# Optimization experiments

Hardware: AMD Instinct MI355X
Metric: run time of the kernel (lower is better)

## Reference

```python
import jax, jax.numpy as jnp
import numpy as np

XYZ, DIRS, APP = 63, 27, 0
HID, OUT, NLAYERS, SKIPS = 256, 4, 8, (4,)

def _linear_init(key, fan_in, fan_out):
    kw, kb = jax.random.split(key)
    s = 1.0 / np.sqrt(fan_in)
    W = jax.random.uniform(kw, (fan_in, fan_out), jnp.float32, -s, s)
    b = jax.random.uniform(kb, (fan_out,), jnp.float32, -s, s)
    return W, b

def setup_inputs() -> dict:
    key = jax.random.key(0)
    keys = jax.random.split(key, NLAYERS + 2)
    x = jax.random.normal(keys[0], (262144, XYZ + DIRS + APP), jnp.float32)
    d = {"x": x}
    in_dim = XYZ
    for i in range(NLAYERS):
        # skip-concat: layer after a skip index sees hid+xyz inputs
        fan_in = HID + XYZ if (i - 1) in SKIPS else (XYZ if i == 0 else HID)
        W, b = _linear_init(keys[i + 1], fan_in, HID)
        d[f"W{i}"], d[f"b{i}"] = W, b
    Wout, bout = _linear_init(keys[-1], HID, OUT)
    d["Wout"], d["bout"] = Wout, bout
    return d

def reference(x, W0, b0, W1, b1, W2, b2, W3, b3, W4, b4, W5, b5, W6, b6, W7, b7, Wout, bout):
    Ws = [W0, W1, W2, W3, W4, W5, W6, W7]
    bs = [b0, b1, b2, b3, b4, b5, b6, b7]
    input_pts = x[..., :XYZ]  # dirs/app split off but unused (use_viewdirs=False)
    h = input_pts
    for i in range(NLAYERS):
        h = jax.nn.relu(h @ Ws[i] + bs[i])
        if i in SKIPS:
            h = jnp.concatenate([input_pts, h], axis=-1)
    return h @ Wout + bout  # [N, 4] = rgb + density logits
```

## Files before the change

### kernel.cpp

```cpp
#include <hip/hip_runtime.h>


typedef _Float16 h8 __attribute__((ext_vector_type(8)));
typedef float f4 __attribute__((ext_vector_type(4)));

#define OFF_L0   0
#define OFF_L1   16384
#define OFF_L2   81920
#define OFF_L3   147456
#define OFF_L4   212992
#define OFF_L5   278528
#define OFF_L6   360448
#define OFF_L7   425984
#define OFF_OUT  491520
#define TOT_HALVES 495616
#define TOT_GROUPS (TOT_HALVES / 8)

__global__ void nerf_prep(const float* __restrict__ W0, const float* __restrict__ W1,
                          const float* __restrict__ W2, const float* __restrict__ W3,
                          const float* __restrict__ W4, const float* __restrict__ W5,
                          const float* __restrict__ W6, const float* __restrict__ W7,
                          const float* __restrict__ Wout, _Float16* __restrict__ wf)
{
    int g = blockIdx.x * 256 + threadIdx.x;
    if (g >= TOT_GROUPS) return;

    const int bounds[10] = {0, 2048, 10240, 18432, 26624, 34816, 45056, 53248, 61440, 61952};
    const float* Ws[9] = {W0, W1, W2, W3, W4, W5, W6, W7, Wout};

    int L = 0;
    while (L < 8 && g >= bounds[L + 1]) ++L;

    int t    = g - bounds[L];
    int lane = t & 63;
    int q    = t >> 6;
    int NF   = (L == 8) ? 1 : 16;
    int nf   = q % NF;
    int ks   = q / NF;
    int n    = nf * 16 + (lane & 15);
    int k0   = ks * 32 + (lane >> 4) * 8;

    const float* W = Ws[L];
    h8 v;
#pragma unroll
    for (int i = 0; i < 8; ++i) {
        int k = k0 + i;
        float val = 0.f;
        if (L == 0) {
            if (k < 63) val = W[k * 256 + n];
        } else if (L == 5) {
            if (k < 256)            val = W[(63 + k) * 256 + n];
            else if ((k - 256) < 63) val = W[(k - 256) * 256 + n];
        } else if (L == 8) {
            if (n < 4) val = W[k * 4 + n];
        } else {
            val = W[k * 256 + n];
        }
        v[i] = (_Float16)val;
    }
    *(h8*)(wf + (size_t)g * 8) = v;
}

__device__ __forceinline__ const h8* bfrag_ptr(const _Float16* __restrict__ w,
                                               int ks, int wid, int nf, int lane)
{
    return (const h8*)(w + (size_t)((ks * 16 + (wid * 4 + nf)) * 64 + lane) * 8);
}

__device__ __forceinline__ void barrier_nodrain()
{
    asm volatile("s_waitcnt lgkmcnt(0)" ::: "memory");
    __builtin_amdgcn_s_barrier();
    __builtin_amdgcn_sched_barrier(0);
}

template <int KSTEPS, int MODE, int GB3, bool LAST>
__device__ __forceinline__ void mlp_layer(_Float16 (&hbuf)[64][264], _Float16 (&xbuf)[64][72],
                                          const _Float16* __restrict__ wfrag,
                                          const _Float16* __restrict__ wnext,
                                          const float* __restrict__ bias,
                                          int wid, int lane, h8 (&pf)[3][4])
{
    const int lg = lane >> 4, ln = lane & 15;

    f4 bv[4];
#pragma unroll
    for (int cf = 0; cf < 4; ++cf)
        bv[cf] = *(const f4*)&bias[wid * 64 + cf * 16 + lg * 4];

    f4 acc[4][4];
#pragma unroll
    for (int cf = 0; cf < 4; ++cf)
#pragma unroll
        for (int sf = 0; sf < 4; ++sf)
            acc[cf][sf] = bv[cf];

#pragma unroll
    for (int ks = 0; ks < KSTEPS; ++ks) {
        const int slot = (GB3 + ks) % 3;
        __builtin_amdgcn_s_setprio(1);
        h8 hfr[4];
#pragma unroll
        for (int sf = 0; sf < 4; ++sf) {
            const _Float16* ap;
            if constexpr (MODE == 1) {
                ap = &xbuf[sf * 16 + ln][ks * 32 + lg * 8];
            } else if constexpr (MODE == 2) {
                ap = (ks < 8) ? &hbuf[sf * 16 + ln][ks * 32 + lg * 8]
                              : &xbuf[sf * 16 + ln][(ks - 8) * 32 + lg * 8];
            } else {
                ap = &hbuf[sf * 16 + ln][ks * 32 + lg * 8];
            }
            hfr[sf] = *(const h8*)ap;
        }
#pragma unroll
        for (int cf = 0; cf < 4; ++cf)
#pragma unroll
            for (int sf = 0; sf < 4; ++sf)
                acc[cf][sf] = __builtin_amdgcn_mfma_f32_16x16x32_f16(pf[slot][cf], hfr[sf], acc[cf][sf], 0, 0, 0);
        __builtin_amdgcn_s_setprio(0);
        if (ks + 3 < KSTEPS) {
#pragma unroll
            for (int cf = 0; cf < 4; ++cf)
                pf[slot][cf] = *bfrag_ptr(wfrag, ks + 3, wid, cf, lane);
        } else if (!LAST) {
#pragma unroll
            for (int cf = 0; cf < 4; ++cf)
                pf[slot][cf] = *bfrag_ptr(wnext, ks + 3 - KSTEPS, wid, cf, lane);
        }
    }

    barrier_nodrain();

#pragma unroll
    for (int cf = 0; cf < 4; ++cf) {
#pragma unroll
        for (int sf = 0; sf < 4; ++sf) {
            union { _Float16 h[4]; unsigned long long u; } p;
#pragma unroll
            for (int i = 0; i < 4; ++i)
                p.h[i] = (_Float16)fmaxf(acc[cf][sf][i], 0.f);
            *(unsigned long long*)&hbuf[sf * 16 + ln][wid * 64 + cf * 16 + lg * 4] = p.u;
        }
    }
    barrier_nodrain();
}

__global__ __launch_bounds__(256, 3) void nerf_fused(
    const float* __restrict__ x,
    const float* __restrict__ b0, const float* __restrict__ b1, const float* __restrict__ b2,
    const float* __restrict__ b3, const float* __restrict__ b4, const float* __restrict__ b5,
    const float* __restrict__ b6, const float* __restrict__ b7, const float* __restrict__ bout,
    const _Float16* __restrict__ wf,
    float* __restrict__ out)
{
    __shared__ _Float16 hbuf[64][264];
    __shared__ _Float16 xbuf[64][72];

    const int tid  = threadIdx.x;
    const int wid  = tid >> 6;
    const int lane = tid & 63;
    const int lg   = lane >> 4, ln = lane & 15;
    const int row0 = blockIdx.x * 64;

    h8 pf[3][4];
#pragma unroll
    for (int cf = 0; cf < 4; ++cf) {
        pf[0][cf] = *bfrag_ptr(wf + OFF_L0, 0, wid, cf, lane);
        pf[1][cf] = *bfrag_ptr(wf + OFF_L0, 1, wid, cf, lane);
        pf[2][cf] = *bfrag_ptr(wf + OFF_L1, 0, wid, cf, lane);
    }

    for (int idx = tid; idx < 64 * 64; idx += 256) {
        int r = idx >> 6, c = idx & 63;
        float v = (c < 63) ? x[(size_t)(row0 + r) * 90 + c] : 0.f;
        xbuf[r][c] = (_Float16)v;
    }
    barrier_nodrain();

    mlp_layer<2,  1, 0, false>(hbuf, xbuf, wf + OFF_L0, wf + OFF_L1, b0, wid, lane, pf);
    mlp_layer<8,  0, 2, false>(hbuf, xbuf, wf + OFF_L1, wf + OFF_L2, b1, wid, lane, pf);
    mlp_layer<8,  0, 1, false>(hbuf, xbuf, wf + OFF_L2, wf + OFF_L3, b2, wid, lane, pf);
    mlp_layer<8,  0, 0, false>(hbuf, xbuf, wf + OFF_L3, wf + OFF_L4, b3, wid, lane, pf);
    mlp_layer<8,  0, 2, false>(hbuf, xbuf, wf + OFF_L4, wf + OFF_L5, b4, wid, lane, pf);
    mlp_layer<10, 2, 1, false>(hbuf, xbuf, wf + OFF_L5, wf + OFF_L6, b5, wid, lane, pf);
    mlp_layer<8,  0, 2, false>(hbuf, xbuf, wf + OFF_L6, wf + OFF_L7, b6, wid, lane, pf);
    mlp_layer<8,  0, 1, true >(hbuf, xbuf, wf + OFF_L7, wf + OFF_L7, b7, wid, lane, pf);

    f4 oacc;
#pragma unroll
    for (int i = 0; i < 4; ++i) oacc[i] = 0.f;
#pragma unroll
    for (int ks = 0; ks < 8; ++ks) {
        h8 bfr = *(const h8*)(wf + OFF_OUT + (size_t)(ks * 64 + lane) * 8);
        h8 afr = *(const h8*)&hbuf[wid * 16 + ln][ks * 32 + lg * 8];
        oacc = __builtin_amdgcn_mfma_f32_16x16x32_f16(afr, bfr, oacc, 0, 0, 0);
    }
    if (ln < 4) {
        float bo = bout[ln];
#pragma unroll
        for (int i = 0; i < 4; ++i) {
            int r = row0 + wid * 16 + lg * 4 + i;
            out[(size_t)r * 4 + ln] = oacc[i] + bo;
        }
    }
}

extern "C" void kernel_launch(void* const* d_in, const int* in_sizes, int n_in,
                              void* d_out, int out_size, void* d_ws, size_t ws_size,
                              hipStream_t stream)
{
    const float* x = (const float*)d_in[0];
    const float* W[9];
    const float* b[9];
    for (int i = 0; i < 8; ++i) {
        W[i] = (const float*)d_in[1 + 2 * i];
        b[i] = (const float*)d_in[2 + 2 * i];
    }
    W[8] = (const float*)d_in[17];
    b[8] = (const float*)d_in[18];

    _Float16* wf = (_Float16*)d_ws;

    nerf_prep<<<(TOT_GROUPS + 255) / 256, 256, 0, stream>>>(
        W[0], W[1], W[2], W[3], W[4], W[5], W[6], W[7], W[8], wf);

    nerf_fused<<<262144 / 64, 256, 0, stream>>>(
        x, b[0], b[1], b[2], b[3], b[4], b[5], b[6], b[7], b[8], wf,
        (float*)d_out);
}
```

Before: 234.9 us.

## Ping-pong activation buffers to drop the mid-layer barrier

Activations now alternate between two shared-memory buffers per layer, so each layer reads one and writes the other. This removes the barrier between a layer's MFMA reads and its writeback. Layer 0 reads only xbuf, so it writes hb[0] in place, and the output head reads hb[1]. The doubled LDS footprint lowers the occupancy hint from 3 to 2 blocks per CU, which cuts latency hiding in exchange for one fewer barrier per layer.

New measurement: 241.2 us. +2.7%, slower.

```diff
diff --git a/kernel.cpp b/kernel.cpp
--- a/kernel.cpp
+++ b/kernel.cpp
@@ -49,7 +49,7 @@
         if (L == 0) {
             if (k < 63) val = W[k * 256 + n];
         } else if (L == 5) {
-            if (k < 256)            val = W[(63 + k) * 256 + n];
+            if (k < 256)             val = W[(63 + k) * 256 + n];
             else if ((k - 256) < 63) val = W[(k - 256) * 256 + n];
         } else if (L == 8) {
             if (n < 4) val = W[k * 4 + n];
@@ -75,7 +75,9 @@
 }
 
 template <int KSTEPS, int MODE, int GB3, bool LAST>
-__device__ __forceinline__ void mlp_layer(_Float16 (&hbuf)[64][264], _Float16 (&xbuf)[64][72],
+__device__ __forceinline__ void mlp_layer(const _Float16 (&rbuf)[64][264],
+                                          _Float16 (&wbuf)[64][264],
+                                          const _Float16 (&xbuf)[64][72],
                                           const _Float16* __restrict__ wfrag,
                                           const _Float16* __restrict__ wnext,
                                           const float* __restrict__ bias,
@@ -106,10 +108,10 @@
             if constexpr (MODE == 1) {
                 ap = &xbuf[sf * 16 + ln][ks * 32 + lg * 8];
             } else if constexpr (MODE == 2) {
-                ap = (ks < 8) ? &hbuf[sf * 16 + ln][ks * 32 + lg * 8]
+                ap = (ks < 8) ? &rbuf[sf * 16 + ln][ks * 32 + lg * 8]
                               : &xbuf[sf * 16 + ln][(ks - 8) * 32 + lg * 8];
             } else {
-                ap = &hbuf[sf * 16 + ln][ks * 32 + lg * 8];
+                ap = &rbuf[sf * 16 + ln][ks * 32 + lg * 8];
             }
             hfr[sf] = *(const h8*)ap;
         }
@@ -123,14 +125,14 @@
 #pragma unroll
             for (int cf = 0; cf < 4; ++cf)
                 pf[slot][cf] = *bfrag_ptr(wfrag, ks + 3, wid, cf, lane);
-        } else if (!LAST) {
-#pragma unroll
-            for (int cf = 0; cf < 4; ++cf)
-                pf[slot][cf] = *bfrag_ptr(wnext, ks + 3 - KSTEPS, wid, cf, lane);
-        }
-    }
-
-    barrier_nodrain();
+        } else {
+            if constexpr (!LAST) {
+#pragma unroll
+                for (int cf = 0; cf < 4; ++cf)
+                    pf[slot][cf] = *bfrag_ptr(wnext, ks + 3 - KSTEPS, wid, cf, lane);
+            }
+        }
+    }
 
 #pragma unroll
     for (int cf = 0; cf < 4; ++cf) {
@@ -140,13 +142,13 @@
 #pragma unroll
             for (int i = 0; i < 4; ++i)
                 p.h[i] = (_Float16)fmaxf(acc[cf][sf][i], 0.f);
-            *(unsigned long long*)&hbuf[sf * 16 + ln][wid * 64 + cf * 16 + lg * 4] = p.u;
+            *(unsigned long long*)&wbuf[sf * 16 + ln][wid * 64 + cf * 16 + lg * 4] = p.u;
         }
     }
     barrier_nodrain();
 }
 
-__global__ __launch_bounds__(256, 3) void nerf_fused(
+__global__ __launch_bounds__(256, 2) void nerf_fused(
     const float* __restrict__ x,
     const float* __restrict__ b0, const float* __restrict__ b1, const float* __restrict__ b2,
     const float* __restrict__ b3, const float* __restrict__ b4, const float* __restrict__ b5,
@@ -154,7 +156,7 @@
     const _Float16* __restrict__ wf,
     float* __restrict__ out)
 {
-    __shared__ _Float16 hbuf[64][264];
+    __shared__ _Float16 hb[2][64][264];
     __shared__ _Float16 xbuf[64][72];
 
     const int tid  = threadIdx.x;
@@ -178,14 +180,14 @@
     }
     barrier_nodrain();
 
-    mlp_layer<2,  1, 0, false>(hbuf, xbuf, wf + OFF_L0, wf + OFF_L1, b0, wid, lane, pf);
-    mlp_layer<8,  0, 2, false>(hbuf, xbuf, wf + OFF_L1, wf + OFF_L2, b1, wid, lane, pf);
-    mlp_layer<8,  0, 1, false>(hbuf, xbuf, wf + OFF_L2, wf + OFF_L3, b2, wid, lane, pf);
-    mlp_layer<8,  0, 0, false>(hbuf, xbuf, wf + OFF_L3, wf + OFF_L4, b3, wid, lane, pf);
-    mlp_layer<8,  0, 2, false>(hbuf, xbuf, wf + OFF_L4, wf + OFF_L5, b4, wid, lane, pf);
-    mlp_layer<10, 2, 1, false>(hbuf, xbuf, wf + OFF_L5, wf + OFF_L6, b5, wid, lane, pf);
-    mlp_layer<8,  0, 2, false>(hbuf, xbuf, wf + OFF_L6, wf + OFF_L7, b6, wid, lane, pf);
-    mlp_layer<8,  0, 1, true >(hbuf, xbuf, wf + OFF_L7, wf + OFF_L7, b7, wid, lane, pf);
+    mlp_layer<2,  1, 0, false>(hb[0], hb[0], xbuf, wf + OFF_L0, wf + OFF_L1, b0, wid, lane, pf);
+    mlp_layer<8,  0, 2, false>(hb[0], hb[1], xbuf, wf + OFF_L1, wf + OFF_L2, b1, wid, lane, pf);
+    mlp_layer<8,  0, 1, false>(hb[1], hb[0], xbuf, wf + OFF_L2, wf + OFF_L3, b2, wid, lane, pf);
+    mlp_layer<8,  0, 0, false>(hb[0], hb[1], xbuf, wf + OFF_L3, wf + OFF_L4, b3, wid, lane, pf);
+    mlp_layer<8,  0, 2, false>(hb[1], hb[0], xbuf, wf + OFF_L4, wf + OFF_L5, b4, wid, lane, pf);
+    mlp_layer<10, 2, 1, false>(hb[0], hb[1], xbuf, wf + OFF_L5, wf + OFF_L6, b5, wid, lane, pf);
+    mlp_layer<8,  0, 2, false>(hb[1], hb[0], xbuf, wf + OFF_L6, wf + OFF_L7, b6, wid, lane, pf);
+    mlp_layer<8,  0, 1, true >(hb[0], hb[1], xbuf, wf + OFF_L7, wf + OFF_L7, b7, wid, lane, pf);
 
     f4 oacc;
 #pragma unroll
@@ -193,7 +195,7 @@
 #pragma unroll
     for (int ks = 0; ks < 8; ++ks) {
         h8 bfr = *(const h8*)(wf + OFF_OUT + (size_t)(ks * 64 + lane) * 8);
-        h8 afr = *(const h8*)&hbuf[wid * 16 + ln][ks * 32 + lg * 8];
+        h8 afr = *(const h8*)&hb[1][wid * 16 + ln][ks * 32 + lg * 8];
         oacc = __builtin_amdgcn_mfma_f32_16x16x32_f16(afr, bfr, oacc, 0, 0, 0);
     }
     if (ln < 4) {
```
